# Optimization experiments

Measured on AMD Instinct MI355X. Metric: run time of the kernel, lower is better.

Reference implementation:

```python
import jax, jax.numpy as jnp
import numpy as np

EMBED = 512
HID = 512
MAXMEM = 65536
THRESH = 0.5
EPS = 1e-12  # F.normalize eps


def setup_inputs() -> dict:
    key = jax.random.key(0)
    ks = jax.random.split(key, 10)
    s = 1.0 / np.sqrt(HID)
    return {
        "keys": jax.random.normal(ks[0], (2, 1024, EMBED), jnp.float32),
        "values": jax.random.normal(ks[1], (2, 1024, EMBED), jnp.float32),
        "attention_scores": jax.random.uniform(ks[2], (2, 1024), jnp.float32),
        "query_embeddings": jax.random.normal(ks[3], (256, EMBED), jnp.float32),
        "keys_mem": jnp.zeros((MAXMEM, EMBED), jnp.float32),
        "values_mem": jnp.zeros((MAXMEM, EMBED), jnp.float32),
        "W_ih": jax.random.uniform(ks[4], (4 * HID, EMBED), jnp.float32, -s, s),
        "W_hh": jax.random.uniform(ks[5], (4 * HID, HID), jnp.float32, -s, s),
        "b_ih": jax.random.uniform(ks[6], (4 * HID,), jnp.float32, -s, s),
        "b_hh": jax.random.uniform(ks[7], (4 * HID,), jnp.float32, -s, s),
        "W_out": jax.random.uniform(ks[8], (EMBED, HID), jnp.float32, -s, s),
        "b_out": jnp.zeros((EMBED,), jnp.float32),
        "top_k": 8,
    }


def _lstm(xs, W_ih, W_hh, b_ih, b_hh):
    # single-layer LSTM over sequence xs: (N, E) -> (N, H), torch gate order i,f,g,o
    H = W_hh.shape[1]
    b = b_ih + b_hh
    def step(carry, x):
        h, c = carry
        g = x @ W_ih.T + h @ W_hh.T + b  # (4H,)
        i, f, gg, o = jnp.split(g, 4)
        c = jax.nn.sigmoid(f) * c + jax.nn.sigmoid(i) * jnp.tanh(gg)
        h = jax.nn.sigmoid(o) * jnp.tanh(c)
        return (h, c), h
    h0 = jnp.zeros((H,), xs.dtype)
    (_, _), hs = jax.lax.scan(step, (h0, h0), xs)
    return hs


def reference(keys, values, attention_scores, query_embeddings, keys_mem, values_mem,
              W_ih, W_hh, b_ih, b_hh, W_out, b_out, top_k):
    E = keys.shape[-1]
    M = keys_mem.shape[0]
    k_flat = keys.reshape(-1, E)
    v_flat = values.reshape(-1, E)
    s_flat = attention_scores.reshape(-1)
    N = k_flat.shape[0]

    # --- update_memory: compact selected tokens to the front (stable), run LSTM,
    # then circular-buffer scatter of the first n_sel outputs (write_index starts at 0).
    mask = s_flat > THRESH
    order = jnp.argsort(jnp.logical_not(mask), stable=True)  # selected first, order preserved
    n_sel = jnp.sum(mask)
    ks = k_flat[order]
    vs = v_flat[order]
    hs = _lstm(ks, W_ih, W_hh, b_ih, b_hh)       # (N, H); first n_sel rows match LSTM on compacted seq
    mem_out = hs @ W_out.T + b_out               # (N, E)

    pos = jnp.arange(N)
    idx = jnp.where(pos < n_sel, pos % M, M)     # M = out-of-range sentinel -> dropped
    keys_mem = keys_mem.at[idx].set(mem_out, mode='drop')
    values_mem = values_mem.at[idx].set(vs, mode='drop')
    current_size = jnp.minimum(n_sel, M)

    # --- retrieve_memory: cosine-similarity top-k over the valid prefix of the bank.
    qn = query_embeddings / jnp.maximum(
        jnp.linalg.norm(query_embeddings, axis=1, keepdims=True), EPS)
    kn = keys_mem / jnp.maximum(jnp.linalg.norm(keys_mem, axis=1, keepdims=True), EPS)
    sims = qn @ kn.T                              # (B, M)
    valid = jnp.arange(M)[None, :] < current_size
    sims = jnp.where(valid, sims, -jnp.inf)
    _, topk_idx = jax.lax.top_k(sims, top_k)      # (B, top_k)
    retrieved = values_mem[topk_idx]              # (B, top_k, E)
    return retrieved
```

## Files before the change

kernel.cpp:

```cpp
#include <hip/hip_runtime.h>
#include <math.h>

#define SENT 2.0f
#define NTOK 2048
#define EDIM 512
#define GJ   2048
#define NW   32
#define HPW  16
#define LOG2E 1.4426950408889634f

typedef float f32x4 __attribute__((ext_vector_type(4)));

__device__ __forceinline__ float sigm_f(float x) {
  return __builtin_amdgcn_rcpf(1.f + __builtin_amdgcn_exp2f(-LOG2E * x));
}
__device__ __forceinline__ float tanh_f(float x) {
  return 1.f - 2.f * __builtin_amdgcn_rcpf(1.f + __builtin_amdgcn_exp2f(2.f * LOG2E * x));
}

__global__ __launch_bounds__(256) void k_init(float4* __restrict__ H4) {
  int i = blockIdx.x * blockDim.x + threadIdx.x;
  H4[i] = make_float4(SENT, SENT, SENT, SENT);
}

__global__ __launch_bounds__(1024) void k_compact(const float* __restrict__ scores,
                                                  int* __restrict__ sel,
                                                  int* __restrict__ nselp) {
  __shared__ int cnt[1024];
  const int tid = threadIdx.x;
  const int i0 = tid * 2, i1 = tid * 2 + 1;
  const int m0 = (scores[i0] > 0.5f) ? 1 : 0;
  const int m1 = (scores[i1] > 0.5f) ? 1 : 0;
  cnt[tid] = m0 + m1;
  __syncthreads();
  for (int off = 1; off < 1024; off <<= 1) {
    int v = cnt[tid];
    int u = (tid >= off) ? cnt[tid - off] : 0;
    __syncthreads();
    cnt[tid] = v + u;
    __syncthreads();
  }
  int excl = (tid == 0) ? 0 : cnt[tid - 1];
  if (m0) sel[excl] = i0;
  if (m1) sel[excl + m0] = i1;
  if (tid == 1023) *nselp = cnt[1023];
}

template<bool GATHER>
__global__ __launch_bounds__(256) void k_gemm(
    const float* __restrict__ A, const float* __restrict__ B,
    const float* __restrict__ bias1, const float* __restrict__ bias2,
    float* __restrict__ C, const int* __restrict__ sel,
    const int* __restrict__ nselp, int J)
{
  const int n_sel = *nselp;
  const int t0 = blockIdx.x * 32;
  if (t0 >= n_sel) return;
  const int j0 = blockIdx.y * 64;
  const int tid = threadIdx.x;
  __shared__ float As[32][36];
  __shared__ float Bst[32][68];
  __shared__ int rowsrc[32];
  if (tid < 32) {
    int t = t0 + tid;
    int r = -1;
    if (t < n_sel) r = GATHER ? sel[t] : t;
    rowsrc[tid] = r;
  }
  __syncthreads();
  const int tx = tid & 15;
  const int ty = tid >> 4;
  float4 acc0 = make_float4(0.f, 0.f, 0.f, 0.f);
  float4 acc1 = make_float4(0.f, 0.f, 0.f, 0.f);
  for (int e0 = 0; e0 < EDIM; e0 += 32) {
    {
      int t = tid >> 3, e4 = tid & 7;
      int r = rowsrc[t];
      float4 v = make_float4(0.f, 0.f, 0.f, 0.f);
      if (r >= 0) v = ((const float4*)(A + (size_t)r * EDIM + e0))[e4];
      *(float4*)&As[t][e4 * 4] = v;
    }
    #pragma unroll
    for (int l = 0; l < 2; ++l) {
      int idx = tid + l * 256;
      int j = idx >> 3, e4 = idx & 7;
      float4 v = ((const float4*)(B + (size_t)(j0 + j) * EDIM + e0))[e4];
      Bst[e4 * 4 + 0][j] = v.x; Bst[e4 * 4 + 1][j] = v.y;
      Bst[e4 * 4 + 2][j] = v.z; Bst[e4 * 4 + 3][j] = v.w;
    }
    __syncthreads();
    #pragma unroll
    for (int e = 0; e < 32; ++e) {
      float a0 = As[ty * 2 + 0][e];
      float a1 = As[ty * 2 + 1][e];
      float4 b = *(const float4*)&Bst[e][tx * 4];
      acc0.x += a0 * b.x; acc0.y += a0 * b.y; acc0.z += a0 * b.z; acc0.w += a0 * b.w;
      acc1.x += a1 * b.x; acc1.y += a1 * b.y; acc1.z += a1 * b.z; acc1.w += a1 * b.w;
    }
    __syncthreads();
  }
  float4 bv = ((const float4*)bias1)[(j0 >> 2) + tx];
  if (bias2) {
    float4 b2 = ((const float4*)bias2)[(j0 >> 2) + tx];
    bv.x += b2.x; bv.y += b2.y; bv.z += b2.z; bv.w += b2.w;
  }
  #pragma unroll
  for (int i = 0; i < 2; ++i) {
    int t = t0 + ty * 2 + i;
    if (t < n_sel) {
      float4 a = (i == 0) ? acc0 : acc1;
      float4 r = make_float4(a.x + bv.x, a.y + bv.y, a.z + bv.z, a.w + bv.w);
      *(float4*)(C + (size_t)t * J + j0 + tx * 4) = r;
    }
  }
}

__global__ __launch_bounds__(512, 1) void k_lstm(
    const float* __restrict__ Gin, float* __restrict__ Hout,
    const float* __restrict__ Whh, const int* __restrict__ nselp)
{
  const int tid = threadIdx.x;
  const int n_sel = *nselp;
  if (n_sel <= 0) return;
  const int w = blockIdx.x;

  const int row_local = tid >> 3;
  const int sub = tid & 7;
  const int g = row_local & 3;
  const int jl = row_local >> 2;
  const int grow = g * 512 + w * HPW + jl;
  const int c0 = sub * 64;
  float4 wv[16];
  {
    const float4* wp = (const float4*)(Whh + (size_t)grow * 512 + c0);
    #pragma unroll
    for (int k = 0; k < 16; ++k) wv[k] = wp[(k + sub) & 15];
  }

  const bool gatel = (tid & 31) == 0;
  const int u = tid >> 5;
  const bool pol = (tid & 1) && (tid < 256);
  const int q = pol ? ((tid - 1) >> 1) : -1;
  const bool pact = pol && (q < 4 * w || q >= 4 * w + 4);

  __shared__ float hbuf[2][512];
  hbuf[0][tid] = 0.f;
  float cst = 0.f;
  float gx0 = 0.f, gx1 = 0.f, gx2 = 0.f, gx3 = 0.f;
  if (gatel) {
    const float* gr = Gin + w * HPW + u;
    gx0 = gr[0]; gx1 = gr[512]; gx2 = gr[1024]; gx3 = gr[1536];
  }
  for (int t = 0; t < n_sel; ++t) {
    const int cur = t & 1;
    float nx0 = 0.f, nx1 = 0.f, nx2 = 0.f, nx3 = 0.f;
    if (gatel && t + 1 < n_sel) {
      const float* gr = Gin + (size_t)(t + 1) * GJ + w * HPW + u;
      nx0 = gr[0]; nx1 = gr[512]; nx2 = gr[1024]; nx3 = gr[1536];
    }
    if (t > 0 && pact) {
      const float* src = Hout + (size_t)(t - 1) * 512 + q * 4;
      float a0, a1, a2, a3, b0, b1, b2, b3, m;
      asm volatile(
        "global_load_dword %[a0], %[s], off sc0 sc1\n\t"
        "global_load_dword %[a1], %[s], off offset:4 sc0 sc1\n\t"
        "global_load_dword %[a2], %[s], off offset:8 sc0 sc1\n\t"
        "global_load_dword %[a3], %[s], off offset:12 sc0 sc1\n\t"
        "global_load_dword %[b0], %[s], off sc0 sc1\n\t"
        "global_load_dword %[b1], %[s], off offset:4 sc0 sc1\n\t"
        "global_load_dword %[b2], %[s], off offset:8 sc0 sc1\n\t"
        "global_load_dword %[b3], %[s], off offset:12 sc0 sc1\n\t"
        "PL%=:\n\t"
        "s_waitcnt vmcnt(4)\n\t"
        "v_max3_f32 %[m], %[a0], %[a1], %[a2]\n\t"
        "v_max_f32 %[m], %[m], %[a3]\n\t"
        "v_cmp_lt_f32 vcc, 1.5, %[m]\n\t"
        "s_cbranch_vccz GA%=\n\t"
        "global_load_dword %[a0], %[s], off sc0 sc1\n\t"
        "global_load_dword %[a1], %[s], off offset:4 sc0 sc1\n\t"
        "global_load_dword %[a2], %[s], off offset:8 sc0 sc1\n\t"
        "global_load_dword %[a3], %[s], off offset:12 sc0 sc1\n\t"
        "s_waitcnt vmcnt(4)\n\t"
        "v_max3_f32 %[m], %[b0], %[b1], %[b2]\n\t"
        "v_max_f32 %[m], %[m], %[b3]\n\t"
        "v_cmp_lt_f32 vcc, 1.5, %[m]\n\t"
        "s_cbranch_vccz GB%=\n\t"
        "global_load_dword %[b0], %[s], off sc0 sc1\n\t"
        "global_load_dword %[b1], %[s], off offset:4 sc0 sc1\n\t"
        "global_load_dword %[b2], %[s], off offset:8 sc0 sc1\n\t"
        "global_load_dword %[b3], %[s], off offset:12 sc0 sc1\n\t"
        "s_branch PL%=\n\t"
        "GB%=:\n\t"
        "s_waitcnt vmcnt(0)\n\t"
        "v_mov_b32 %[a0], %[b0]\n\t"
        "v_mov_b32 %[a1], %[b1]\n\t"
        "v_mov_b32 %[a2], %[b2]\n\t"
        "v_mov_b32 %[a3], %[b3]\n\t"
        "GA%=:\n\t"
        "s_waitcnt vmcnt(0)\n\t"
        : [a0]"=&v"(a0), [a1]"=&v"(a1), [a2]"=&v"(a2), [a3]"=&v"(a3),
          [b0]"=&v"(b0), [b1]"=&v"(b1), [b2]"=&v"(b2), [b3]"=&v"(b3),
          [m]"=&v"(m)
        : [s]"v"(src)
        : "vcc", "memory");
      hbuf[cur][q * 4 + 0] = a0; hbuf[cur][q * 4 + 1] = a1;
      hbuf[cur][q * 4 + 2] = a2; hbuf[cur][q * 4 + 3] = a3;
    }
    __syncthreads();
    const float4* hv = (const float4*)&hbuf[cur][c0];
    float s0 = 0.f, s1 = 0.f, s2 = 0.f, s3 = 0.f;
    #pragma unroll
    for (int k = 0; k < 4; ++k) {
      float4 w4, h4;
      w4 = wv[4*k+0]; h4 = hv[(4*k+0+sub)&15]; s0 += w4.x*h4.x + w4.y*h4.y + w4.z*h4.z + w4.w*h4.w;
      w4 = wv[4*k+1]; h4 = hv[(4*k+1+sub)&15]; s1 += w4.x*h4.x + w4.y*h4.y + w4.z*h4.z + w4.w*h4.w;
      w4 = wv[4*k+2]; h4 = hv[(4*k+2+sub)&15]; s2 += w4.x*h4.x + w4.y*h4.y + w4.z*h4.z + w4.w*h4.w;
      w4 = wv[4*k+3]; h4 = hv[(4*k+3+sub)&15]; s3 += w4.x*h4.x + w4.y*h4.y + w4.z*h4.z + w4.w*h4.w;
    }
    float s = (s0 + s1) + (s2 + s3);
    s += __shfl_xor(s, 1); s += __shfl_xor(s, 2); s += __shfl_xor(s, 4);
    const int lane = tid & 63;
    float sf = __shfl(s, lane + 8);
    float sg = __shfl(s, lane + 16);
    float so = __shfl(s, lane + 24);
    if (gatel) {
      float gi = gx0 + s;
      float gf = gx1 + sf;
      float gg = gx2 + sg;
      float go = gx3 + so;
      float ig = sigm_f(gi);
      float fg = sigm_f(gf);
      float og = sigm_f(go);
      cst = fg * cst + ig * tanh_f(gg);
      float h = og * tanh_f(cst);
      __hip_atomic_store(Hout + (size_t)t * 512 + w * HPW + u, h,
                         __ATOMIC_RELAXED, __HIP_MEMORY_SCOPE_AGENT);
      hbuf[cur ^ 1][w * HPW + u] = h;
      gx0 = nx0; gx1 = nx1; gx2 = nx2; gx3 = nx3;
    }
  }
}

__global__ __launch_bounds__(256) void k_norms(
    const float* __restrict__ memo, const float* __restrict__ qe,
    float* __restrict__ dens, const int* __restrict__ nselp)
{
  const int n_sel = *nselp;
  const int row = blockIdx.x * 4 + (threadIdx.x >> 6);
  const int lane = threadIdx.x & 63;
  const float* src;
  if (row < NTOK) {
    if (row >= n_sel) return;
    src = memo + (size_t)row * EDIM;
  } else {
    if (row >= NTOK + 256) return;
    src = qe + (size_t)(row - NTOK) * EDIM;
  }
  const float4* s4 = (const float4*)src;
  float4 a = s4[lane], b = s4[lane + 64];
  float s = a.x*a.x + a.y*a.y + a.z*a.z + a.w*a.w
          + b.x*b.x + b.y*b.y + b.z*b.z + b.w*b.w;
  #pragma unroll
  for (int off = 32; off; off >>= 1) s += __shfl_xor(s, off);
  if (lane == 0) dens[row] = fmaxf(sqrtf(s), 1e-12f);
}

__global__ __launch_bounds__(256) void k_retrieve(
    const float* __restrict__ memo, const float* __restrict__ qe,
    const float* __restrict__ dens, const float* __restrict__ values,
    const int* __restrict__ sel, const int* __restrict__ nselp,
    float* __restrict__ out, int top_k)
{
  const int n_sel = *nselp;
  const int qb = blockIdx.x * 4;
  const int tid = threadIdx.x;
  __shared__ float qs[4][EDIM];
  __shared__ float sims[4][NTOK];
  __shared__ int tix[4][8];
  for (int l = tid; l < 512; l += 256) {
    int q = l >> 7, e4 = l & 127;
    float4 v = ((const float4*)(qe + (size_t)(qb + q) * EDIM))[e4];
    float inv = 1.f / dens[NTOK + qb + q];
    v.x *= inv; v.y *= inv; v.z *= inv; v.w *= inv;
    *(float4*)&qs[q][e4 * 4] = v;
  }
  __syncthreads();
  for (int t = tid; t < n_sel; t += 256) {
    const float4* m4 = (const float4*)(memo + (size_t)t * EDIM);
    float a0 = 0.f, a1 = 0.f, a2 = 0.f, a3 = 0.f;
    for (int e4 = 0; e4 < 128; ++e4) {
      float4 m = m4[e4];
      float4 q0 = *(const float4*)&qs[0][e4 * 4];
      float4 q1 = *(const float4*)&qs[1][e4 * 4];
      float4 q2 = *(const float4*)&qs[2][e4 * 4];
      float4 q3 = *(const float4*)&qs[3][e4 * 4];
      a0 += m.x*q0.x + m.y*q0.y + m.z*q0.z + m.w*q0.w;
      a1 += m.x*q1.x + m.y*q1.y + m.z*q1.z + m.w*q1.w;
      a2 += m.x*q2.x + m.y*q2.y + m.z*q2.z + m.w*q2.w;
      a3 += m.x*q3.x + m.y*q3.y + m.z*q3.z + m.w*q3.w;
    }
    float inv = 1.f / dens[t];
    sims[0][t] = a0 * inv; sims[1][t] = a1 * inv;
    sims[2][t] = a2 * inv; sims[3][t] = a3 * inv;
  }
  __syncthreads();
  const int wq = tid >> 6, lane = tid & 63;
  for (int r = 0; r < top_k; ++r) {
    if (r < n_sel) {
      float bv = -INFINITY; int bi = 0x7fffffff;
      for (int t = lane; t < n_sel; t += 64) {
        float v = sims[wq][t];
        if (v > bv || (v == bv && t < bi)) { bv = v; bi = t; }
      }
      #pragma unroll
      for (int off = 32; off; off >>= 1) {
        float ov = __shfl_xor(bv, off);
        int   oi = __shfl_xor(bi, off);
        if (ov > bv || (ov == bv && oi < bi)) { bv = ov; bi = oi; }
      }
      if (lane == 0) { tix[wq][r] = bi; sims[wq][bi] = -INFINITY; }
    } else if (lane == 0) {
      tix[wq][r] = -1;
    }
    __syncthreads();
  }
  const int tot = 4 * top_k * 128;
  for (int l = tid; l < tot; l += 256) {
    int q = l / (top_k * 128);
    int rem = l - q * top_k * 128;
    int r = rem >> 7;
    int e4 = rem & 127;
    int t = tix[q][r];
    float4 v = make_float4(0.f, 0.f, 0.f, 0.f);
    if (t >= 0) v = ((const float4*)(values + (size_t)sel[t] * EDIM))[e4];
    ((float4*)out)[(((size_t)(qb + q) * top_k) + r) * 128 + e4] = v;
  }
}

extern "C" void kernel_launch(void* const* d_in, const int* in_sizes, int n_in,
                              void* d_out, int out_size, void* d_ws, size_t ws_size,
                              hipStream_t stream) {
  const float* keys   = (const float*)d_in[0];
  const float* values = (const float*)d_in[1];
  const float* scores = (const float*)d_in[2];
  const float* qe     = (const float*)d_in[3];
  const float* W_ih   = (const float*)d_in[6];
  const float* W_hh   = (const float*)d_in[7];
  const float* b_ih   = (const float*)d_in[8];
  const float* b_hh   = (const float*)d_in[9];
  const float* W_out  = (const float*)d_in[10];
  const float* b_out  = (const float*)d_in[11];
  float* out = (float*)d_out;
  const int top_k = out_size / (256 * 512);

  char* ws = (char*)d_ws;
  int*   nsel   = (int*)ws;
  int*   sel    = (int*)(ws + 4096);
  float* dens   = (float*)(ws + 16384);
  float* Hout   = (float*)(ws + (size_t)(1u << 20));
  float* Gin    = (float*)(ws + (size_t)(9u << 20));
  float* memo   = (float*)(ws + (size_t)(9u << 20));
  (void)in_sizes; (void)n_in; (void)ws_size;

  k_init<<<1024, 256, 0, stream>>>((float4*)Hout);
  k_compact<<<1, 1024, 0, stream>>>(scores, sel, nsel);
  k_gemm<true ><<<dim3(64, 32), 256, 0, stream>>>(keys, W_ih, b_ih, b_hh, Gin, sel, nsel, GJ);
  k_lstm<<<NW, 512, 0, stream>>>(Gin, Hout, W_hh, nsel);
  k_gemm<false><<<dim3(64, 8), 256, 0, stream>>>(Hout, W_out, b_out, nullptr, memo, nullptr, nsel, EDIM);
  k_norms<<<576, 256, 0, stream>>>(memo, qe, dens, nsel);
  k_retrieve<<<64, 256, 0, stream>>>(memo, qe, dens, values, sel, nsel, out, top_k);
}
```

Before: 1.826 ms.

## Split LSTM block into dedicated poller waves and compute waves, relax load cache bits

```diff
diff --git a/kernel.cpp b/kernel.cpp
--- a/kernel.cpp
+++ b/kernel.cpp
@@ -115,7 +115,7 @@
   }
 }
 
-__global__ __launch_bounds__(512, 1) void k_lstm(
+__global__ __launch_bounds__(640, 1) void k_lstm(
     const float* __restrict__ Gin, float* __restrict__ Hout,
     const float* __restrict__ Whh, const int* __restrict__ nselp)
 {
@@ -124,27 +124,31 @@
   if (n_sel <= 0) return;
   const int w = blockIdx.x;
 
-  const int row_local = tid >> 3;
-  const int sub = tid & 7;
+  const int dt = tid - 128;
+  const int row_local = dt >> 3;
+  const int sub = dt & 7;
   const int g = row_local & 3;
   const int jl = row_local >> 2;
-  const int grow = g * 512 + w * HPW + jl;
   const int c0 = sub * 64;
-  float4 wv[16];
-  {
-    const float4* wp = (const float4*)(Whh + (size_t)grow * 512 + c0);
+
+  f32x4 wv[16];
+  if (dt >= 0) {
+    const int grow = g * 512 + w * HPW + jl;
+    const f32x4* wp = (const f32x4*)(Whh + (size_t)grow * 512 + c0);
     #pragma unroll
     for (int k = 0; k < 16; ++k) wv[k] = wp[(k + sub) & 15];
-  }
-
-  const bool gatel = (tid & 31) == 0;
-  const int u = tid >> 5;
-  const bool pol = (tid & 1) && (tid < 256);
-  const int q = pol ? ((tid - 1) >> 1) : -1;
-  const bool pact = pol && (q < 4 * w || q >= 4 * w + 4);
+    #pragma unroll
+    for (int k = 0; k < 16; ++k)
+      asm volatile("" : "+v"(wv[k]));
+  }
+
+  const int q = (tid < 128) ? tid : -1;
+  const bool pact = (q >= 0) && (q < 4 * w || q >= 4 * w + 4);
+  const bool gatel = (dt >= 0) && ((dt & 31) == 0);
+  const int u = dt >> 5;
 
   __shared__ float hbuf[2][512];
-  hbuf[0][tid] = 0.f;
+  if (tid < 512) hbuf[0][tid] = 0.f;
   float cst = 0.f;
   float gx0 = 0.f, gx1 = 0.f, gx2 = 0.f, gx3 = 0.f;
   if (gatel) {
@@ -162,33 +166,33 @@
       const float* src = Hout + (size_t)(t - 1) * 512 + q * 4;
       float a0, a1, a2, a3, b0, b1, b2, b3, m;
       asm volatile(
-        "global_load_dword %[a0], %[s], off sc0 sc1\n\t"
-        "global_load_dword %[a1], %[s], off offset:4 sc0 sc1\n\t"
-        "global_load_dword %[a2], %[s], off offset:8 sc0 sc1\n\t"
-        "global_load_dword %[a3], %[s], off offset:12 sc0 sc1\n\t"
-        "global_load_dword %[b0], %[s], off sc0 sc1\n\t"
-        "global_load_dword %[b1], %[s], off offset:4 sc0 sc1\n\t"
-        "global_load_dword %[b2], %[s], off offset:8 sc0 sc1\n\t"
-        "global_load_dword %[b3], %[s], off offset:12 sc0 sc1\n\t"
+        "global_load_dword %[a0], %[s], off sc1\n\t"
+        "global_load_dword %[a1], %[s], off offset:4 sc1\n\t"
+        "global_load_dword %[a2], %[s], off offset:8 sc1\n\t"
+        "global_load_dword %[a3], %[s], off offset:12 sc1\n\t"
+        "global_load_dword %[b0], %[s], off sc1\n\t"
+        "global_load_dword %[b1], %[s], off offset:4 sc1\n\t"
+        "global_load_dword %[b2], %[s], off offset:8 sc1\n\t"
+        "global_load_dword %[b3], %[s], off offset:12 sc1\n\t"
         "PL%=:\n\t"
         "s_waitcnt vmcnt(4)\n\t"
         "v_max3_f32 %[m], %[a0], %[a1], %[a2]\n\t"
         "v_max_f32 %[m], %[m], %[a3]\n\t"
         "v_cmp_lt_f32 vcc, 1.5, %[m]\n\t"
         "s_cbranch_vccz GA%=\n\t"
-        "global_load_dword %[a0], %[s], off sc0 sc1\n\t"
-        "global_load_dword %[a1], %[s], off offset:4 sc0 sc1\n\t"
-        "global_load_dword %[a2], %[s], off offset:8 sc0 sc1\n\t"
-        "global_load_dword %[a3], %[s], off offset:12 sc0 sc1\n\t"
+        "global_load_dword %[a0], %[s], off sc1\n\t"
+        "global_load_dword %[a1], %[s], off offset:4 sc1\n\t"
+        "global_load_dword %[a2], %[s], off offset:8 sc1\n\t"
+        "global_load_dword %[a3], %[s], off offset:12 sc1\n\t"
         "s_waitcnt vmcnt(4)\n\t"
         "v_max3_f32 %[m], %[b0], %[b1], %[b2]\n\t"
         "v_max_f32 %[m], %[m], %[b3]\n\t"
         "v_cmp_lt_f32 vcc, 1.5, %[m]\n\t"
         "s_cbranch_vccz GB%=\n\t"
-        "global_load_dword %[b0], %[s], off sc0 sc1\n\t"
-        "global_load_dword %[b1], %[s], off offset:4 sc0 sc1\n\t"
-        "global_load_dword %[b2], %[s], off offset:8 sc0 sc1\n\t"
-        "global_load_dword %[b3], %[s], off offset:12 sc0 sc1\n\t"
+        "global_load_dword %[b0], %[s], off sc1\n\t"
+        "global_load_dword %[b1], %[s], off offset:4 sc1\n\t"
+        "global_load_dword %[b2], %[s], off offset:8 sc1\n\t"
+        "global_load_dword %[b3], %[s], off offset:12 sc1\n\t"
         "s_branch PL%=\n\t"
         "GB%=:\n\t"
         "s_waitcnt vmcnt(0)\n\t"
@@ -207,36 +211,38 @@
       hbuf[cur][q * 4 + 2] = a2; hbuf[cur][q * 4 + 3] = a3;
     }
     __syncthreads();
-    const float4* hv = (const float4*)&hbuf[cur][c0];
-    float s0 = 0.f, s1 = 0.f, s2 = 0.f, s3 = 0.f;
-    #pragma unroll
-    for (int k = 0; k < 4; ++k) {
-      float4 w4, h4;
-      w4 = wv[4*k+0]; h4 = hv[(4*k+0+sub)&15]; s0 += w4.x*h4.x + w4.y*h4.y + w4.z*h4.z + w4.w*h4.w;
-      w4 = wv[4*k+1]; h4 = hv[(4*k+1+sub)&15]; s1 += w4.x*h4.x + w4.y*h4.y + w4.z*h4.z + w4.w*h4.w;
-      w4 = wv[4*k+2]; h4 = hv[(4*k+2+sub)&15]; s2 += w4.x*h4.x + w4.y*h4.y + w4.z*h4.z + w4.w*h4.w;
-      w4 = wv[4*k+3]; h4 = hv[(4*k+3+sub)&15]; s3 += w4.x*h4.x + w4.y*h4.y + w4.z*h4.z + w4.w*h4.w;
-    }
-    float s = (s0 + s1) + (s2 + s3);
-    s += __shfl_xor(s, 1); s += __shfl_xor(s, 2); s += __shfl_xor(s, 4);
-    const int lane = tid & 63;
-    float sf = __shfl(s, lane + 8);
-    float sg = __shfl(s, lane + 16);
-    float so = __shfl(s, lane + 24);
-    if (gatel) {
-      float gi = gx0 + s;
-      float gf = gx1 + sf;
-      float gg = gx2 + sg;
-      float go = gx3 + so;
-      float ig = sigm_f(gi);
-      float fg = sigm_f(gf);
-      float og = sigm_f(go);
-      cst = fg * cst + ig * tanh_f(gg);
-      float h = og * tanh_f(cst);
-      __hip_atomic_store(Hout + (size_t)t * 512 + w * HPW + u, h,
-                         __ATOMIC_RELAXED, __HIP_MEMORY_SCOPE_AGENT);
-      hbuf[cur ^ 1][w * HPW + u] = h;
-      gx0 = nx0; gx1 = nx1; gx2 = nx2; gx3 = nx3;
+    if (dt >= 0) {
+      const f32x4* hv = (const f32x4*)&hbuf[cur][c0];
+      float s0 = 0.f, s1 = 0.f, s2 = 0.f, s3 = 0.f;
+      #pragma unroll
+      for (int k = 0; k < 4; ++k) {
+        f32x4 w4, h4;
+        w4 = wv[4*k+0]; h4 = hv[(4*k+0+sub)&15]; s0 += w4[0]*h4[0] + w4[1]*h4[1] + w4[2]*h4[2] + w4[3]*h4[3];
+        w4 = wv[4*k+1]; h4 = hv[(4*k+1+sub)&15]; s1 += w4[0]*h4[0] + w4[1]*h4[1] + w4[2]*h4[2] + w4[3]*h4[3];
+        w4 = wv[4*k+2]; h4 = hv[(4*k+2+sub)&15]; s2 += w4[0]*h4[0] + w4[1]*h4[1] + w4[2]*h4[2] + w4[3]*h4[3];
+        w4 = wv[4*k+3]; h4 = hv[(4*k+3+sub)&15]; s3 += w4[0]*h4[0] + w4[1]*h4[1] + w4[2]*h4[2] + w4[3]*h4[3];
+      }
+      float s = (s0 + s1) + (s2 + s3);
+      s += __shfl_xor(s, 1); s += __shfl_xor(s, 2); s += __shfl_xor(s, 4);
+      const int lane = dt & 63;
+      float sf = __shfl(s, lane + 8);
+      float sg = __shfl(s, lane + 16);
+      float so = __shfl(s, lane + 24);
+      if (gatel) {
+        float gi = gx0 + s;
+        float gf = gx1 + sf;
+        float gg = gx2 + sg;
+        float go = gx3 + so;
+        float ig = sigm_f(gi);
+        float fg = sigm_f(gf);
+        float og = sigm_f(go);
+        cst = fg * cst + ig * tanh_f(gg);
+        float h = og * tanh_f(cst);
+        __hip_atomic_store(Hout + (size_t)t * 512 + w * HPW + u, h,
+                           __ATOMIC_RELAXED, __HIP_MEMORY_SCOPE_AGENT);
+        hbuf[cur ^ 1][w * HPW + u] = h;
+        gx0 = nx0; gx1 = nx1; gx2 = nx2; gx3 = nx3;
+      }
     }
   }
 }
@@ -365,7 +371,7 @@
   k_init<<<1024, 256, 0, stream>>>((float4*)Hout);
   k_compact<<<1, 1024, 0, stream>>>(scores, sel, nsel);
   k_gemm<true ><<<dim3(64, 32), 256, 0, stream>>>(keys, W_ih, b_ih, b_hh, Gin, sel, nsel, GJ);
-  k_lstm<<<NW, 512, 0, stream>>>(Gin, Hout, W_hh, nsel);
+  k_lstm<<<NW, 640, 0, stream>>>(Gin, Hout, W_hh, nsel);
   k_gemm<false><<<dim3(64, 8), 256, 0, stream>>>(Hout, W_out, b_out, nullptr, memo, nullptr, nsel, EDIM);
   k_norms<<<576, 256, 0, stream>>>(memo, qe, dens, nsel);
   k_retrieve<<<64, 256, 0, stream>>>(memo, qe, dens, values, sel, nsel, out, top_k);
```

Measured after the change: 3.996 ms. 2.19x slower.
